# Performance work log

Measured on AMD Instinct MI355X. Metric: run time of the kernel, lower is better.

The kernel has to match this reference:

```python
import jax, jax.numpy as jnp
import numpy as np

N, K, CIN, COUT = 150000, 27, 128, 128


def setup_inputs() -> dict:
    key = jax.random.key(0)
    k1, k2, k3 = jax.random.split(key, 3)
    data = jax.random.normal(k1, (N, CIN), dtype=jnp.float32)
    weights = jax.random.normal(k2, (COUT, K, CIN), dtype=jnp.float32) * 0.05
    # neighbour indices in [-1, N): -1 marks empty octree neighbours (~1/151 here)
    neighbour = jax.random.randint(k3, (N, K), 0, N + 1, dtype=jnp.int64) - 1
    return {"data": data, "weights": weights, "neighbour": neighbour}


def reference(data, weights, neighbour):
    """Octree sparse conv: out[m] = sum_k W[:,k,:] @ data[neigh[m,k]] (0 if -1).

    Scans over the 27 kernel offsets so the [N,K,Cin] gather is never
    materialized; each step is a masked row-gather + dense GEMM.
    """
    w_k = jnp.transpose(weights, (1, 2, 0))   # [K, Cin, Cout]
    n_k = neighbour.T                          # [K, N]

    def body(acc, xs):
        w, idx = xs                            # [Cin, Cout], [N]
        valid = (idx >= 0)[:, None]            # [N, 1]
        g = jnp.where(valid, data[jnp.clip(idx, 0, None)], 0.0)  # [N, Cin]
        return acc + g @ w, None

    out0 = jnp.zeros((data.shape[0], w_k.shape[-1]), dtype=data.dtype)
    out, _ = jax.lax.scan(body, out0, (w_k, n_k))
    return out
```

## Files before the change

### kernel.cpp

```cpp
#include <hip/hip_runtime.h>

#define N_PTS 150000
#define NK 27
#define CIN 128
#define COUT 128
#define BM 256
#define NBLK ((N_PTS + BM - 1) / BM)

typedef __attribute__((ext_vector_type(8))) short bfrag8;
typedef __attribute__((ext_vector_type(4))) float facc4;

__device__ inline unsigned short f2bf(float f) {
    unsigned u = __builtin_bit_cast(unsigned, f);
    u += 0x7FFFu + ((u >> 16) & 1u);
    return (unsigned short)(u >> 16);
}
__device__ inline unsigned pack2(float a, float b) {
    return (unsigned)f2bf(a) | ((unsigned)f2bf(b) << 16);
}
__device__ inline void glds16(const void* g, void* l) {
    __builtin_amdgcn_global_load_lds(
        (const __attribute__((address_space(1))) void*)g,
        (__attribute__((address_space(3))) void*)l, 16, 0, 0);
}
__device__ inline void phase_barrier() {
    __builtin_amdgcn_sched_barrier(0);
    asm volatile("s_waitcnt vmcnt(0)" ::: "memory");
    __builtin_amdgcn_s_barrier();
    __builtin_amdgcn_sched_barrier(0);
}

__global__ void cast_data_kernel(const float* __restrict__ in,
                                 unsigned short* __restrict__ out) {
    const int n8_data = N_PTS * (CIN / 8);
    const int n8_all  = (N_PTS + 1) * (CIN / 8);
    int i = blockIdx.x * blockDim.x + threadIdx.x;
    int stride = gridDim.x * blockDim.x;
    for (; i < n8_all; i += stride) {
        uint4 v;
        if (i < n8_data) {
            const float4* p = (const float4*)(in + (size_t)i * 8);
            float4 x = p[0], y = p[1];
            v.x = pack2(x.x, x.y); v.y = pack2(x.z, x.w);
            v.z = pack2(y.x, y.y); v.w = pack2(y.z, y.w);
        } else {
            v.x = v.y = v.z = v.w = 0u;
        }
        *(uint4*)(out + (size_t)i * 8) = v;
    }
}

__global__ void prep_weights_h(const float* __restrict__ w,
                               unsigned short* __restrict__ wkh) {
    int i = blockIdx.x * blockDim.x + threadIdx.x;
    if (i >= NK * 2 * 128 * 8) return;
    int bu = i & 7, co = (i >> 3) & 127, h = (i >> 10) & 1, k = i >> 11;
    int ci = h * 64 + (bu ^ (co & 7)) * 8;
    const float4* src = (const float4*)(w + ((size_t)co * NK + k) * CIN + ci);
    float4 x = src[0], y = src[1];
    uint4 v;
    v.x = pack2(x.x, x.y); v.y = pack2(x.z, x.w);
    v.z = pack2(y.x, y.y); v.w = pack2(y.z, y.w);
    ((uint4*)wkh)[i] = v;
}


#define STAGE(K2H, HB, ADST0, ADST1, BDST)                                          \
  {                                                                                 \
    glds16(wkhB + (size_t)(K2H) * 16384 + bsrc_c, BDST);                            \
    int iv0 = *(const int*)(ldsI + i0base + ((K2H) >> 1) * 4);                      \
    int iv1 = *(const int*)(ldsI + i1base + ((K2H) >> 1) * 4);                      \
    size_t e0 = (r0ok && iv0 >= 0) ? (size_t)iv0 : (size_t)N_PTS;                   \
    size_t e1 = (r1ok && iv1 >= 0) ? (size_t)iv1 : (size_t)N_PTS;                   \
    glds16(dbfB + e0 * 256 + (HB) + aswz0, ADST0);                                  \
    glds16(dbfB + e1 * 256 + (HB) + aswz1, ADST1);                                  \
  }

#define MFMA_PHASE(ABUF, BBUF)                                                      \
  {                                                                                 \
    __builtin_amdgcn_s_setprio(1);                                                  \
    _Pragma("unroll")                                                               \
    for (int kk = 0; kk < 2; ++kk) {                                                \
      const int sw_ = (((kk * 4 + lk) ^ (lr & 7)) << 4);                            \
      bfrag8 a0 = *(const bfrag8*)((ABUF) + (wrow * 32 + lr) * 128 + sw_);          \
      bfrag8 a1 = *(const bfrag8*)((ABUF) + (wrow * 32 + 16 + lr) * 128 + sw_);     \
      _Pragma("unroll")                                                             \
      for (int ct = 0; ct < 4; ++ct) {                                              \
        bfrag8 b = *(const bfrag8*)((BBUF) + (h * 64 + ct * 16 + lr) * 128 + sw_);  \
        acc[0][ct] = __builtin_amdgcn_mfma_f32_16x16x32_bf16(a0, b, acc[0][ct],     \
                                                             0, 0, 0);              \
        acc[1][ct] = __builtin_amdgcn_mfma_f32_16x16x32_bf16(a1, b, acc[1][ct],     \
                                                             0, 0, 0);              \
      }                                                                             \
    }                                                                               \
    __builtin_amdgcn_s_setprio(0);                                                  \
  }

__global__ __launch_bounds__(1024, 4)
void octconv_v5(const unsigned short* __restrict__ dbf,
                const unsigned short* __restrict__ wkh,
                const int* __restrict__ nbr,
                float* __restrict__ out) {
    __shared__ __align__(1024) unsigned char lds[98304 + 27648];

    const int t = threadIdx.x;
    const int w = t >> 6, l = t & 63;
    const int lr = l & 15, lk = l >> 4;
    const int h = w & 1, wrow = w >> 1;
    const int m0 = blockIdx.x * BM;

    const int lu    = l & 7;
    const int slot0 = w * 16 + (l >> 3);
    const int slot1 = slot0 + 8;
    const bool r0ok = (m0 + slot0) < N_PTS;
    const bool r1ok = (m0 + slot1) < N_PTS;
    const int aswz0 = (lu ^ (slot0 & 7)) << 4;
    const int aswz1 = (lu ^ (slot1 & 7)) << 4;
    const int bco   = w * 8 + (l >> 3);
    const int bsrc_c = ((bco * 8 + (l & 7)) << 4);
    const int i0base = slot0 * 108;
    const int i1base = slot1 * 108;

    const char* dbfB = (const char*)dbf;
    const char* wkhB = (const char*)wkh;
    char* ldsA0 = (char*)lds;
    char* ldsA1 = (char*)lds + 32768;
    char* ldsB0 = (char*)lds + 65536;
    char* ldsB1 = (char*)lds + 81920;
    char* ldsI  = (char*)lds + 98304;

    char* adst0_0 = ldsA0 + (w * 128 + l) * 16;
    char* adst0_1 = ldsA0 + (w * 128 + 64 + l) * 16;
    char* adst1_0 = ldsA1 + (w * 128 + l) * 16;
    char* adst1_1 = ldsA1 + (w * 128 + 64 + l) * 16;
    char* bdst0   = ldsB0 + t * 16;
    char* bdst1   = ldsB1 + t * 16;

    facc4 acc[2][4];
    const facc4 fz = {0.f, 0.f, 0.f, 0.f};
#pragma unroll
    for (int a = 0; a < 2; ++a)
#pragma unroll
        for (int b = 0; b < 4; ++b) acc[a][b] = fz;

    {
        const char* nsrc = (const char*)nbr + (size_t)m0 * 108;
        const int rows_valid = (N_PTS - m0) < BM ? (N_PTS - m0) : BM;
        const int nlimit = rows_valid * 108;
        int o1 = t * 16;
        if (o1 < nlimit) glds16(nsrc + o1, ldsI + o1);
        int o2 = 16384 + t * 16;
        if (t < 704 && o2 < nlimit) glds16(nsrc + o2, ldsI + o2);
        glds16(wkhB + bsrc_c, bdst0);
    }
    phase_barrier();
    {
        int iv0 = *(const int*)(ldsI + i0base);
        int iv1 = *(const int*)(ldsI + i1base);
        size_t e0 = (r0ok && iv0 >= 0) ? (size_t)iv0 : (size_t)N_PTS;
        size_t e1 = (r1ok && iv1 >= 0) ? (size_t)iv1 : (size_t)N_PTS;
        glds16(dbfB + e0 * 256 + aswz0, adst0_0);
        glds16(dbfB + e1 * 256 + aswz1, adst0_1);
    }
    phase_barrier();

#pragma unroll 1
    for (int kp = 0; kp < NK; ++kp) {
        STAGE(2 * kp + 1, 128, adst1_0, adst1_1, bdst1)
        MFMA_PHASE(ldsA0, ldsB0)
        phase_barrier();
        if (kp + 1 < NK) {
            STAGE(2 * kp + 2, 0, adst0_0, adst0_1, bdst0)
            MFMA_PHASE(ldsA1, ldsB1)
            phase_barrier();
        } else {
            MFMA_PHASE(ldsA1, ldsB1)
        }
    }

#pragma unroll
    for (int rt = 0; rt < 2; ++rt) {
        const int r0 = m0 + wrow * 32 + rt * 16 + lk * 4;
#pragma unroll
        for (int ct = 0; ct < 4; ++ct) {
#pragma unroll
            for (int r = 0; r < 4; ++r) {
                int row = r0 + r;
                if (row < N_PTS)
                    out[(size_t)row * COUT + h * 64 + ct * 16 + lr] = acc[rt][ct][r];
            }
        }
    }
}

__global__ void naive_kernel(const float* __restrict__ data, const float* __restrict__ wgt,
                             const int* __restrict__ nbr, float* __restrict__ out) {
    int mm = blockIdx.x;
    int co = threadIdx.x;
    if (mm >= N_PTS) return;
    float acc = 0.f;
    for (int k = 0; k < NK; ++k) {
        int idx = nbr[mm * NK + k];
        if (idx < 0) continue;
        const float* d  = data + (size_t)idx * CIN;
        const float* wp = wgt + ((size_t)co * NK + k) * CIN;
        for (int ci = 0; ci < CIN; ++ci) acc += d[ci] * wp[ci];
    }
    out[(size_t)mm * COUT + co] = acc;
}

extern "C" void kernel_launch(void* const* d_in, const int* in_sizes, int n_in,
                              void* d_out, int out_size, void* d_ws, size_t ws_size,
                              hipStream_t stream) {
    const float* data = (const float*)d_in[0];
    const float* wgt  = (const float*)d_in[1];
    const int*   nbr  = (const int*)d_in[2];
    float*       out  = (float*)d_out;

    const size_t wk_bytes  = (size_t)NK * 2 * 128 * 8 * 16;
    const size_t dbf_bytes = (size_t)(N_PTS + 1) * CIN * 2;

    if (ws_size < wk_bytes + dbf_bytes) {
        naive_kernel<<<N_PTS, COUT, 0, stream>>>(data, wgt, nbr, out);
        return;
    }
    unsigned short* wkh = (unsigned short*)d_ws;
    unsigned short* dbf = (unsigned short*)((char*)d_ws + wk_bytes);

    prep_weights_h<<<(NK * 2 * 128 * 8 + 255) / 256, 256, 0, stream>>>(wgt, wkh);
    cast_data_kernel<<<2048, 256, 0, stream>>>(data, dbf);

    octconv_v5<<<NBLK, 1024, 0, stream>>>(dbf, wkh, nbr, out);
}
```

Measured before the change: 203.2 us.

## Stage gathers through registers with two-deep prefetch and LDS-only barriers

Replaces the direct global-to-LDS gather loads with ordinary global loads into registers, issued two half-stages ahead. The registers are then written to the double-buffered LDS tiles after the MFMA phase. Barriers now wait only on LDS counters instead of draining all outstanding global loads, so gather latency can overlap more MFMA work. The cost is extra VGPRs, explicit LDS write instructions, and a clamped redundant load and write on the final iteration.

```diff
diff --git a/kernel.cpp b/kernel.cpp
--- a/kernel.cpp
+++ b/kernel.cpp
@@ -23,9 +23,16 @@
         (const __attribute__((address_space(1))) void*)g,
         (__attribute__((address_space(3))) void*)l, 16, 0, 0);
 }
-__device__ inline void phase_barrier() {
+__device__ inline void lds_barrier() {
+    __builtin_amdgcn_sched_barrier(0);
+    asm volatile("s_waitcnt lgkmcnt(0)" ::: "memory");
+    __builtin_amdgcn_s_barrier();
+    __builtin_amdgcn_sched_barrier(0);
+}
+__device__ inline void full_barrier() {
     __builtin_amdgcn_sched_barrier(0);
     asm volatile("s_waitcnt vmcnt(0)" ::: "memory");
+    asm volatile("s_waitcnt lgkmcnt(0)" ::: "memory");
     __builtin_amdgcn_s_barrier();
     __builtin_amdgcn_sched_barrier(0);
 }
@@ -65,15 +72,25 @@
 }
 
 
-#define STAGE(K2H, HB, ADST0, ADST1, BDST)                                          \
-  {                                                                                 \
-    glds16(wkhB + (size_t)(K2H) * 16384 + bsrc_c, BDST);                            \
-    int iv0 = *(const int*)(ldsI + i0base + ((K2H) >> 1) * 4);                      \
-    int iv1 = *(const int*)(ldsI + i1base + ((K2H) >> 1) * 4);                      \
-    size_t e0 = (r0ok && iv0 >= 0) ? (size_t)iv0 : (size_t)N_PTS;                   \
-    size_t e1 = (r1ok && iv1 >= 0) ? (size_t)iv1 : (size_t)N_PTS;                   \
-    glds16(dbfB + e0 * 256 + (HB) + aswz0, ADST0);                                  \
-    glds16(dbfB + e1 * 256 + (HB) + aswz1, ADST1);                                  \
+#define ISSUE(Q, RA0, RA1, RB)                                             \
+  {                                                                        \
+    const int q_ = (Q) <= 53 ? (Q) : 53;                                   \
+    const int k_ = q_ >> 1;                                                \
+    const int hb_ = (q_ & 1) << 7;                                         \
+    int iv0 = *(const int*)(ldsI + i0base + k_ * 4);                       \
+    int iv1 = *(const int*)(ldsI + i1base + k_ * 4);                       \
+    size_t e0 = (r0ok && iv0 >= 0) ? (size_t)iv0 : (size_t)N_PTS;          \
+    size_t e1 = (r1ok && iv1 >= 0) ? (size_t)iv1 : (size_t)N_PTS;          \
+    RA0 = *(const uint4*)(dbfB + e0 * 256 + hb_ + aswz0);                  \
+    RA1 = *(const uint4*)(dbfB + e1 * 256 + hb_ + aswz1);                  \
+    RB  = *(const uint4*)(wkhB + (size_t)q_ * 16384 + bsrc_c);             \
+  }
+
+#define DSWRITE(ABUF, BBUF, RA0, RA1, RB)                                  \
+  {                                                                        \
+    *(uint4*)((ABUF) + adst_lin0) = RA0;                                   \
+    *(uint4*)((ABUF) + adst_lin1) = RA1;                                   \
+    *(uint4*)((BBUF) + bdst_lin)  = RB;                                    \
   }
 
 #define MFMA_PHASE(ABUF, BBUF)                                                      \
@@ -97,7 +114,7 @@
   }
 
 __global__ __launch_bounds__(1024, 4)
-void octconv_v5(const unsigned short* __restrict__ dbf,
+void octconv_v6(const unsigned short* __restrict__ dbf,
                 const unsigned short* __restrict__ wkh,
                 const int* __restrict__ nbr,
                 float* __restrict__ out) {
@@ -129,12 +146,9 @@
     char* ldsB1 = (char*)lds + 81920;
     char* ldsI  = (char*)lds + 98304;
 
-    char* adst0_0 = ldsA0 + (w * 128 + l) * 16;
-    char* adst0_1 = ldsA0 + (w * 128 + 64 + l) * 16;
-    char* adst1_0 = ldsA1 + (w * 128 + l) * 16;
-    char* adst1_1 = ldsA1 + (w * 128 + 64 + l) * 16;
-    char* bdst0   = ldsB0 + t * 16;
-    char* bdst1   = ldsB1 + t * 16;
+    const int adst_lin0 = (w * 128 + l) * 16;
+    const int adst_lin1 = (w * 128 + 64 + l) * 16;
+    const int bdst_lin  = t * 16;
 
     facc4 acc[2][4];
     const facc4 fz = {0.f, 0.f, 0.f, 0.f};
@@ -151,31 +165,26 @@
         if (o1 < nlimit) glds16(nsrc + o1, ldsI + o1);
         int o2 = 16384 + t * 16;
         if (t < 704 && o2 < nlimit) glds16(nsrc + o2, ldsI + o2);
-        glds16(wkhB + bsrc_c, bdst0);
-    }
-    phase_barrier();
-    {
-        int iv0 = *(const int*)(ldsI + i0base);
-        int iv1 = *(const int*)(ldsI + i1base);
-        size_t e0 = (r0ok && iv0 >= 0) ? (size_t)iv0 : (size_t)N_PTS;
-        size_t e1 = (r1ok && iv1 >= 0) ? (size_t)iv1 : (size_t)N_PTS;
-        glds16(dbfB + e0 * 256 + aswz0, adst0_0);
-        glds16(dbfB + e1 * 256 + aswz1, adst0_1);
-    }
-    phase_barrier();
+    }
+    full_barrier();
+
+    uint4 sa0_0, sa1_0, sb_0;
+    uint4 sa0_1, sa1_1, sb_1;
+    ISSUE(0, sa0_0, sa1_0, sb_0)
+    ISSUE(1, sa0_1, sa1_1, sb_1)
+    DSWRITE(ldsA0, ldsB0, sa0_0, sa1_0, sb_0)
+    lds_barrier();
 
 #pragma unroll 1
     for (int kp = 0; kp < NK; ++kp) {
-        STAGE(2 * kp + 1, 128, adst1_0, adst1_1, bdst1)
+        if (kp < NK - 1) ISSUE(2 * kp + 2, sa0_0, sa1_0, sb_0)
         MFMA_PHASE(ldsA0, ldsB0)
-        phase_barrier();
-        if (kp + 1 < NK) {
-            STAGE(2 * kp + 2, 0, adst0_0, adst0_1, bdst0)
-            MFMA_PHASE(ldsA1, ldsB1)
-            phase_barrier();
-        } else {
-            MFMA_PHASE(ldsA1, ldsB1)
-        }
+        DSWRITE(ldsA1, ldsB1, sa0_1, sa1_1, sb_1)
+        lds_barrier();
+        if (kp < NK - 1) ISSUE(2 * kp + 3, sa0_1, sa1_1, sb_1)
+        MFMA_PHASE(ldsA1, ldsB1)
+        DSWRITE(ldsA0, ldsB0, sa0_0, sa1_0, sb_0)
+        lds_barrier();
     }
 
 #pragma unroll
@@ -230,5 +239,5 @@
     prep_weights_h<<<(NK * 2 * 128 * 8 + 255) / 256, 256, 0, stream>>>(wgt, wkh);
     cast_data_kernel<<<2048, 256, 0, stream>>>(data, dbf);
 
-    octconv_v5<<<NBLK, 1024, 0, stream>>>(dbf, wkh, nbr, out);
-}
+    octconv_v6<<<NBLK, 1024, 0, stream>>>(dbf, wkh, nbr, out);
+}
```

Result: slower. 211.7 us (+4.2%).

## Gather A rows straight into registers and widen per-wave output tile

Applied to the files above, without the earlier changes.

Activation rows are no longer staged through LDS. Each lane loads its MFMA A fragments directly from global memory into registers, double-buffered across the two half-K steps. Blocks drop from 1024 to 512 threads, and each wave now covers all 128 output channels for its 32 rows, so every gathered A fragment feeds twice as many MFMAs and LDS use shrinks. The costs are higher register pressure from 16 accumulators plus 8 uint4 gather buffers, and exposed global-load latency that was previously hidden by the async LDS path.

```diff
diff --git a/kernel.cpp b/kernel.cpp
--- a/kernel.cpp
+++ b/kernel.cpp
@@ -65,129 +65,128 @@
 }
 
 
-#define STAGE(K2H, HB, ADST0, ADST1, BDST)                                          \
-  {                                                                                 \
-    glds16(wkhB + (size_t)(K2H) * 16384 + bsrc_c, BDST);                            \
-    int iv0 = *(const int*)(ldsI + i0base + ((K2H) >> 1) * 4);                      \
-    int iv1 = *(const int*)(ldsI + i1base + ((K2H) >> 1) * 4);                      \
-    size_t e0 = (r0ok && iv0 >= 0) ? (size_t)iv0 : (size_t)N_PTS;                   \
-    size_t e1 = (r1ok && iv1 >= 0) ? (size_t)iv1 : (size_t)N_PTS;                   \
-    glds16(dbfB + e0 * 256 + (HB) + aswz0, ADST0);                                  \
-    glds16(dbfB + e1 * 256 + (HB) + aswz1, ADST1);                                  \
+#define ISSUE_A(SET, IV, HB)                                                 \
+  {                                                                          \
+    size_t e0_ = (r0ok && (IV).x >= 0) ? (size_t)(IV).x : (size_t)N_PTS;     \
+    size_t e1_ = (r1ok && (IV).y >= 0) ? (size_t)(IV).y : (size_t)N_PTS;     \
+    const char* p0_ = dbfB + e0_ * 256 + (HB) + lk * 16;                     \
+    const char* p1_ = dbfB + e1_ * 256 + (HB) + lk * 16;                     \
+    SET##00 = *(const uint4*)(p0_);                                          \
+    SET##01 = *(const uint4*)(p0_ + 64);                                     \
+    SET##10 = *(const uint4*)(p1_);                                          \
+    SET##11 = *(const uint4*)(p1_ + 64);                                     \
   }
 
-#define MFMA_PHASE(ABUF, BBUF)                                                      \
-  {                                                                                 \
-    __builtin_amdgcn_s_setprio(1);                                                  \
-    _Pragma("unroll")                                                               \
-    for (int kk = 0; kk < 2; ++kk) {                                                \
-      const int sw_ = (((kk * 4 + lk) ^ (lr & 7)) << 4);                            \
-      bfrag8 a0 = *(const bfrag8*)((ABUF) + (wrow * 32 + lr) * 128 + sw_);          \
-      bfrag8 a1 = *(const bfrag8*)((ABUF) + (wrow * 32 + 16 + lr) * 128 + sw_);     \
-      _Pragma("unroll")                                                             \
-      for (int ct = 0; ct < 4; ++ct) {                                              \
-        bfrag8 b = *(const bfrag8*)((BBUF) + (h * 64 + ct * 16 + lr) * 128 + sw_);  \
-        acc[0][ct] = __builtin_amdgcn_mfma_f32_16x16x32_bf16(a0, b, acc[0][ct],     \
-                                                             0, 0, 0);              \
-        acc[1][ct] = __builtin_amdgcn_mfma_f32_16x16x32_bf16(a1, b, acc[1][ct],     \
-                                                             0, 0, 0);              \
-      }                                                                             \
-    }                                                                               \
-    __builtin_amdgcn_s_setprio(0);                                                  \
+#define STAGE_B(Q, BBUF)                                                     \
+  {                                                                          \
+    const char* bs_ = wkhB + (size_t)(Q) * 16384 + w * 2048 + l * 16;        \
+    glds16(bs_,        (BBUF) + w * 2048 + l * 16);                          \
+    glds16(bs_ + 1024, (BBUF) + w * 2048 + 1024 + l * 16);                   \
   }
 
-__global__ __launch_bounds__(1024, 4)
-void octconv_v5(const unsigned short* __restrict__ dbf,
+#define MFMA_PHASE(SET, BBUF)                                                        \
+  {                                                                                  \
+    __builtin_amdgcn_s_setprio(1);                                                   \
+    _Pragma("unroll")                                                                \
+    for (int ct = 0; ct < 8; ++ct) {                                                 \
+      const int bro_ = (ct * 16 + lr) * 128;                                         \
+      bfrag8 b0 = *(const bfrag8*)((BBUF) + bro_ + ((lk ^ (lr & 7)) << 4));          \
+      bfrag8 b1 = *(const bfrag8*)((BBUF) + bro_ + (((4 + lk) ^ (lr & 7)) << 4));    \
+      acc[0][ct] = __builtin_amdgcn_mfma_f32_16x16x32_bf16(                          \
+          __builtin_bit_cast(bfrag8, SET##00), b0, acc[0][ct], 0, 0, 0);             \
+      acc[1][ct] = __builtin_amdgcn_mfma_f32_16x16x32_bf16(                          \
+          __builtin_bit_cast(bfrag8, SET##10), b0, acc[1][ct], 0, 0, 0);             \
+      acc[0][ct] = __builtin_amdgcn_mfma_f32_16x16x32_bf16(                          \
+          __builtin_bit_cast(bfrag8, SET##01), b1, acc[0][ct], 0, 0, 0);             \
+      acc[1][ct] = __builtin_amdgcn_mfma_f32_16x16x32_bf16(                          \
+          __builtin_bit_cast(bfrag8, SET##11), b1, acc[1][ct], 0, 0, 0);             \
+    }                                                                                \
+    __builtin_amdgcn_s_setprio(0);                                                   \
+  }
+
+__global__ __launch_bounds__(512, 4)
+void octconv_v7(const unsigned short* __restrict__ dbf,
                 const unsigned short* __restrict__ wkh,
                 const int* __restrict__ nbr,
                 float* __restrict__ out) {
-    __shared__ __align__(1024) unsigned char lds[98304 + 27648];
+    __shared__ __align__(1024) unsigned char lds[32768 + 27648];
 
     const int t = threadIdx.x;
     const int w = t >> 6, l = t & 63;
     const int lr = l & 15, lk = l >> 4;
-    const int h = w & 1, wrow = w >> 1;
     const int m0 = blockIdx.x * BM;
 
-    const int lu    = l & 7;
-    const int slot0 = w * 16 + (l >> 3);
-    const int slot1 = slot0 + 8;
-    const bool r0ok = (m0 + slot0) < N_PTS;
-    const bool r1ok = (m0 + slot1) < N_PTS;
-    const int aswz0 = (lu ^ (slot0 & 7)) << 4;
-    const int aswz1 = (lu ^ (slot1 & 7)) << 4;
-    const int bco   = w * 8 + (l >> 3);
-    const int bsrc_c = ((bco * 8 + (l & 7)) << 4);
-    const int i0base = slot0 * 108;
-    const int i1base = slot1 * 108;
+    const int row0 = m0 + w * 32 + lr;
+    const bool r0ok = row0 < N_PTS;
+    const bool r1ok = (row0 + 16) < N_PTS;
 
     const char* dbfB = (const char*)dbf;
     const char* wkhB = (const char*)wkh;
-    char* ldsA0 = (char*)lds;
-    char* ldsA1 = (char*)lds + 32768;
-    char* ldsB0 = (char*)lds + 65536;
-    char* ldsB1 = (char*)lds + 81920;
-    char* ldsI  = (char*)lds + 98304;
-
-    char* adst0_0 = ldsA0 + (w * 128 + l) * 16;
-    char* adst0_1 = ldsA0 + (w * 128 + 64 + l) * 16;
-    char* adst1_0 = ldsA1 + (w * 128 + l) * 16;
-    char* adst1_1 = ldsA1 + (w * 128 + 64 + l) * 16;
-    char* bdst0   = ldsB0 + t * 16;
-    char* bdst1   = ldsB1 + t * 16;
-
-    facc4 acc[2][4];
+    char* ldsB0 = (char*)lds;
+    char* ldsB1 = (char*)lds + 16384;
+    char* ldsI  = (char*)lds + 32768;
+
+    const int islab0 = (w * 32 + lr) * 108;
+    const int islab1 = (w * 32 + 16 + lr) * 108;
+
+    facc4 acc[2][8];
     const facc4 fz = {0.f, 0.f, 0.f, 0.f};
 #pragma unroll
     for (int a = 0; a < 2; ++a)
 #pragma unroll
-        for (int b = 0; b < 4; ++b) acc[a][b] = fz;
+        for (int b = 0; b < 8; ++b) acc[a][b] = fz;
 
     {
         const char* nsrc = (const char*)nbr + (size_t)m0 * 108;
         const int rows_valid = (N_PTS - m0) < BM ? (N_PTS - m0) : BM;
         const int nlimit = rows_valid * 108;
-        int o1 = t * 16;
-        if (o1 < nlimit) glds16(nsrc + o1, ldsI + o1);
-        int o2 = 16384 + t * 16;
-        if (t < 704 && o2 < nlimit) glds16(nsrc + o2, ldsI + o2);
-        glds16(wkhB + bsrc_c, bdst0);
+        int o;
+        o = t * 16;         if (o < nlimit) glds16(nsrc + o, ldsI + o);
+        o = 8192 + t * 16;  if (o < nlimit) glds16(nsrc + o, ldsI + o);
+        o = 16384 + t * 16; if (o < nlimit) glds16(nsrc + o, ldsI + o);
+        o = 24576 + t * 16; if (t < 192 && o < nlimit) glds16(nsrc + o, ldsI + o);
+        STAGE_B(0, ldsB0)
     }
     phase_barrier();
-    {
-        int iv0 = *(const int*)(ldsI + i0base);
-        int iv1 = *(const int*)(ldsI + i1base);
-        size_t e0 = (r0ok && iv0 >= 0) ? (size_t)iv0 : (size_t)N_PTS;
-        size_t e1 = (r1ok && iv1 >= 0) ? (size_t)iv1 : (size_t)N_PTS;
-        glds16(dbfB + e0 * 256 + aswz0, adst0_0);
-        glds16(dbfB + e1 * 256 + aswz1, adst0_1);
-    }
-    phase_barrier();
+
+    int2 ivC, ivN;
+    ivC.x = *(const int*)(ldsI + islab0);
+    ivC.y = *(const int*)(ldsI + islab1);
+
+    uint4 sx00, sx01, sx10, sx11;
+    uint4 sy00, sy01, sy10, sy11;
+    ISSUE_A(sx, ivC, 0)
 
 #pragma unroll 1
-    for (int kp = 0; kp < NK; ++kp) {
-        STAGE(2 * kp + 1, 128, adst1_0, adst1_1, bdst1)
-        MFMA_PHASE(ldsA0, ldsB0)
+    for (int k = 0; k < NK; ++k) {
+        STAGE_B(2 * k + 1, ldsB1)
+        {
+            const int kn = (k + 1 < NK) ? k + 1 : NK - 1;
+            ivN.x = *(const int*)(ldsI + islab0 + kn * 4);
+            ivN.y = *(const int*)(ldsI + islab1 + kn * 4);
+        }
+        ISSUE_A(sy, ivC, 128)
+        MFMA_PHASE(sx, ldsB0)
         phase_barrier();
-        if (kp + 1 < NK) {
-            STAGE(2 * kp + 2, 0, adst0_0, adst0_1, bdst0)
-            MFMA_PHASE(ldsA1, ldsB1)
-            phase_barrier();
-        } else {
-            MFMA_PHASE(ldsA1, ldsB1)
-        }
+        if (k + 1 < NK) {
+            STAGE_B(2 * k + 2, ldsB0)
+            ISSUE_A(sx, ivN, 0)
+        }
+        MFMA_PHASE(sy, ldsB1)
+        if (k + 1 < NK) phase_barrier();
+        ivC = ivN;
     }
 
 #pragma unroll
     for (int rt = 0; rt < 2; ++rt) {
-        const int r0 = m0 + wrow * 32 + rt * 16 + lk * 4;
-#pragma unroll
-        for (int ct = 0; ct < 4; ++ct) {
+        const int r0 = m0 + w * 32 + rt * 16 + lk * 4;
+#pragma unroll
+        for (int ct = 0; ct < 8; ++ct) {
 #pragma unroll
             for (int r = 0; r < 4; ++r) {
                 int row = r0 + r;
                 if (row < N_PTS)
-                    out[(size_t)row * COUT + h * 64 + ct * 16 + lr] = acc[rt][ct][r];
+                    out[(size_t)row * COUT + ct * 16 + lr] = acc[rt][ct][r];
             }
         }
     }
@@ -230,5 +229,5 @@
     prep_weights_h<<<(NK * 2 * 128 * 8 + 255) / 256, 256, 0, stream>>>(wgt, wkh);
     cast_data_kernel<<<2048, 256, 0, stream>>>(data, dbf);
 
-    octconv_v5<<<NBLK, 1024, 0, stream>>>(dbf, wkh, nbr, out);
-}
+    octconv_v7<<<NBLK, 512, 0, stream>>>(dbf, wkh, nbr, out);
+}
```

Result: slower. 237.3 us (+16.8%).

## Triple-buffer gathered A tiles with partial vmcnt waits for deeper prefetch

Applied to the files above, without the earlier changes.

Replaces the double-buffered A/B staging with a three-deep ring for the gathered activation rows and double buffering for weights. Each phase now waits only until the older loads finish (vmcnt(2)), so the row gather for step p+2 stays in flight while step p computes. The goal is to hide more of the irregular gather latency behind MFMA work. LDS use grows to about 156KB per block, and the correctness of the partial waits depends on the exact ordering of the issued loads.

```diff
diff --git a/kernel.cpp b/kernel.cpp
--- a/kernel.cpp
+++ b/kernel.cpp
@@ -22,12 +22,6 @@
     __builtin_amdgcn_global_load_lds(
         (const __attribute__((address_space(1))) void*)g,
         (__attribute__((address_space(3))) void*)l, 16, 0, 0);
-}
-__device__ inline void phase_barrier() {
-    __builtin_amdgcn_sched_barrier(0);
-    asm volatile("s_waitcnt vmcnt(0)" ::: "memory");
-    __builtin_amdgcn_s_barrier();
-    __builtin_amdgcn_sched_barrier(0);
 }
 
 __global__ void cast_data_kernel(const float* __restrict__ in,
@@ -65,16 +59,21 @@
 }
 
 
-#define STAGE(K2H, HB, ADST0, ADST1, BDST)                                          \
-  {                                                                                 \
-    glds16(wkhB + (size_t)(K2H) * 16384 + bsrc_c, BDST);                            \
-    int iv0 = *(const int*)(ldsI + i0base + ((K2H) >> 1) * 4);                      \
-    int iv1 = *(const int*)(ldsI + i1base + ((K2H) >> 1) * 4);                      \
-    size_t e0 = (r0ok && iv0 >= 0) ? (size_t)iv0 : (size_t)N_PTS;                   \
-    size_t e1 = (r1ok && iv1 >= 0) ? (size_t)iv1 : (size_t)N_PTS;                   \
-    glds16(dbfB + e0 * 256 + (HB) + aswz0, ADST0);                                  \
-    glds16(dbfB + e1 * 256 + (HB) + aswz1, ADST1);                                  \
+#define STAGE_A(Q, ADST)                                                     \
+  {                                                                          \
+    const int q_ = (Q);                                                      \
+    const int k_ = q_ >> 1;                                                  \
+    const int hb_ = (q_ & 1) << 7;                                           \
+    int iv0 = *(const int*)(ldsI + i0base + k_ * 4);                         \
+    int iv1 = *(const int*)(ldsI + i1base + k_ * 4);                         \
+    size_t e0 = (r0ok && iv0 >= 0) ? (size_t)iv0 : (size_t)N_PTS;            \
+    size_t e1 = (r1ok && iv1 >= 0) ? (size_t)iv1 : (size_t)N_PTS;            \
+    glds16(dbfB + e0 * 256 + hb_ + aswz0, (ADST) + adst0);                   \
+    glds16(dbfB + e1 * 256 + hb_ + aswz1, (ADST) + adst1);                   \
   }
+
+#define STAGE_B(Q, BDST)                                                     \
+    glds16(wkhB + (size_t)(Q) * 16384 + bsrc_c, (BDST) + bdst_lin);
 
 #define MFMA_PHASE(ABUF, BBUF)                                                      \
   {                                                                                 \
@@ -96,12 +95,18 @@
     __builtin_amdgcn_s_setprio(0);                                                  \
   }
 
+#define WAIT_BAR(N)                                                          \
+    __builtin_amdgcn_sched_barrier(0);                                       \
+    asm volatile("s_waitcnt vmcnt(" #N ")" ::: "memory");                    \
+    __builtin_amdgcn_s_barrier();                                            \
+    __builtin_amdgcn_sched_barrier(0);
+
 __global__ __launch_bounds__(1024, 4)
-void octconv_v5(const unsigned short* __restrict__ dbf,
+void octconv_v8(const unsigned short* __restrict__ dbf,
                 const unsigned short* __restrict__ wkh,
                 const int* __restrict__ nbr,
                 float* __restrict__ out) {
-    __shared__ __align__(1024) unsigned char lds[98304 + 27648];
+    __shared__ __align__(1024) unsigned char lds[3 * 32768 + 2 * 16384 + 27648];
 
     const int t = threadIdx.x;
     const int w = t >> 6, l = t & 63;
@@ -116,25 +121,21 @@
     const bool r1ok = (m0 + slot1) < N_PTS;
     const int aswz0 = (lu ^ (slot0 & 7)) << 4;
     const int aswz1 = (lu ^ (slot1 & 7)) << 4;
-    const int bco   = w * 8 + (l >> 3);
-    const int bsrc_c = ((bco * 8 + (l & 7)) << 4);
+    const int adst0 = slot0 * 128 + lu * 16;
+    const int adst1 = slot1 * 128 + lu * 16;
+    const int bsrc_c = t * 16;
+    const int bdst_lin = t * 16;
     const int i0base = slot0 * 108;
     const int i1base = slot1 * 108;
 
     const char* dbfB = (const char*)dbf;
     const char* wkhB = (const char*)wkh;
-    char* ldsA0 = (char*)lds;
-    char* ldsA1 = (char*)lds + 32768;
-    char* ldsB0 = (char*)lds + 65536;
-    char* ldsB1 = (char*)lds + 81920;
-    char* ldsI  = (char*)lds + 98304;
-
-    char* adst0_0 = ldsA0 + (w * 128 + l) * 16;
-    char* adst0_1 = ldsA0 + (w * 128 + 64 + l) * 16;
-    char* adst1_0 = ldsA1 + (w * 128 + l) * 16;
-    char* adst1_1 = ldsA1 + (w * 128 + 64 + l) * 16;
-    char* bdst0   = ldsB0 + t * 16;
-    char* bdst1   = ldsB1 + t * 16;
+    char* a0p = (char*)lds;
+    char* a1p = (char*)lds + 32768;
+    char* a2p = (char*)lds + 65536;
+    char* b0p = (char*)lds + 98304;
+    char* b1p = (char*)lds + 114688;
+    char* ldsI = (char*)lds + 131072;
 
     facc4 acc[2][4];
     const facc4 fz = {0.f, 0.f, 0.f, 0.f};
@@ -151,32 +152,38 @@
         if (o1 < nlimit) glds16(nsrc + o1, ldsI + o1);
         int o2 = 16384 + t * 16;
         if (t < 704 && o2 < nlimit) glds16(nsrc + o2, ldsI + o2);
-        glds16(wkhB + bsrc_c, bdst0);
-    }
-    phase_barrier();
-    {
-        int iv0 = *(const int*)(ldsI + i0base);
-        int iv1 = *(const int*)(ldsI + i1base);
-        size_t e0 = (r0ok && iv0 >= 0) ? (size_t)iv0 : (size_t)N_PTS;
-        size_t e1 = (r1ok && iv1 >= 0) ? (size_t)iv1 : (size_t)N_PTS;
-        glds16(dbfB + e0 * 256 + aswz0, adst0_0);
-        glds16(dbfB + e1 * 256 + aswz1, adst0_1);
-    }
-    phase_barrier();
+    }
+    WAIT_BAR(0)
+
+    STAGE_A(0, a0p)
+    STAGE_B(0, b0p)
+    STAGE_A(1, a1p)
+    STAGE_B(1, b1p)
+    WAIT_BAR(3)
+
+    STAGE_A(2, a2p)
+    MFMA_PHASE(a0p, b0p)
+    WAIT_BAR(2)
+    { char* tp = a0p; a0p = a1p; a1p = a2p; a2p = tp; }
+    { char* tp = b0p; b0p = b1p; b1p = tp; }
 
 #pragma unroll 1
-    for (int kp = 0; kp < NK; ++kp) {
-        STAGE(2 * kp + 1, 128, adst1_0, adst1_1, bdst1)
-        MFMA_PHASE(ldsA0, ldsB0)
-        phase_barrier();
-        if (kp + 1 < NK) {
-            STAGE(2 * kp + 2, 0, adst0_0, adst0_1, bdst0)
-            MFMA_PHASE(ldsA1, ldsB1)
-            phase_barrier();
-        } else {
-            MFMA_PHASE(ldsA1, ldsB1)
-        }
-    }
+    for (int p = 1; p <= 51; ++p) {
+        STAGE_B(p + 1, b1p)
+        STAGE_A(p + 2, a2p)
+        MFMA_PHASE(a0p, b0p)
+        WAIT_BAR(2)
+        { char* tp = a0p; a0p = a1p; a1p = a2p; a2p = tp; }
+        { char* tp = b0p; b0p = b1p; b1p = tp; }
+    }
+
+    STAGE_B(53, b1p)
+    MFMA_PHASE(a0p, b0p)
+    WAIT_BAR(0)
+    { char* tp = a0p; a0p = a1p; a1p = a2p; a2p = tp; }
+    { char* tp = b0p; b0p = b1p; b1p = tp; }
+
+    MFMA_PHASE(a0p, b0p)
 
 #pragma unroll
     for (int rt = 0; rt < 2; ++rt) {
@@ -230,5 +237,5 @@
     prep_weights_h<<<(NK * 2 * 128 * 8 + 255) / 256, 256, 0, stream>>>(wgt, wkh);
     cast_data_kernel<<<2048, 256, 0, stream>>>(data, dbf);
 
-    octconv_v5<<<NBLK, 1024, 0, stream>>>(dbf, wkh, nbr, out);
-}
+    octconv_v8<<<NBLK, 1024, 0, stream>>>(dbf, wkh, nbr, out);
+}
```

Result: faster. 197.2 us (-3.0%).
